# Kernel optimization log

Measured on AMD Instinct MI355X. Metric: run time of the kernel, lower is better.

Reference implementation:

```python
import jax, jax.numpy as jnp
import numpy as np

SHIFTS = [1, 3, 5, 7]
C = 16  # in_channels // 4
# -1 neighbor offsets for tmp1..tmp8 (dy, dx) in units of the dilation
OFFSETS = [(-1, -1), (-1, 0), (-1, 1), (0, 1), (1, 1), (1, 0), (1, -1), (0, -1)]


def setup_inputs() -> dict:
    key = jax.random.key(0)
    ks = jax.random.split(key, 32)
    d = {}
    d['cen'] = jax.random.normal(ks[0], (8, 64, 256, 256), jnp.float32)
    d['mas'] = jax.random.normal(ks[1], (8, 1, 256, 256), jnp.float32)
    d['in_conv_w'] = jax.random.normal(ks[2], (16, 64), jnp.float32) * 0.1
    d['in_conv_b'] = jax.random.normal(ks[3], (16,), jnp.float32) * 0.1
    for i, s in enumerate(SHIFTS):
        d[f'dw_w{s}'] = jax.random.normal(ks[4 + 2 * i], (16, 1, s, s), jnp.float32) * 0.1
        d[f'dw_b{s}'] = jax.random.normal(ks[5 + 2 * i], (16,), jnp.float32) * 0.1
    d['l1_w'] = jax.random.normal(ks[12], (4, 16, 4), jnp.float32) * 0.1
    d['l1_b'] = jax.random.normal(ks[13], (4, 16), jnp.float32) * 0.1
    d['l2_w'] = jax.random.normal(ks[14], (4, 16, 8), jnp.float32) * 0.1
    d['l2_b'] = jax.random.normal(ks[15], (4, 16), jnp.float32) * 0.1
    d['base_w'] = jax.random.normal(ks[16], (16, 4), jnp.float32) * 0.1
    d['bn_scale'] = jnp.ones((16,), jnp.float32)
    d['bn_bias'] = jnp.zeros((16,), jnp.float32)
    d['final_w'] = jax.random.normal(ks[17], (1, 16), jnp.float32) * 0.1
    d['final_b'] = jax.random.normal(ks[18], (1,), jnp.float32) * 0.1
    return d


def _dw_conv(x, w, b, pad):
    # depthwise conv, groups == channels
    y = jax.lax.conv_general_dilated(
        x, w, window_strides=(1, 1), padding=[(pad, pad), (pad, pad)],
        dimension_numbers=('NCHW', 'OIHW', 'NCHW'), feature_group_count=x.shape[1])
    return y + b[None, :, None, None]


def _shifted(x, dy, dx, d):
    # zero-padded shift: out(y,x) = in(y+dy, x+dx)
    H, W = x.shape[2], x.shape[3]
    p = jnp.pad(x, ((0, 0), (0, 0), (d, d), (d, d)))
    return p[:, :, d + dy:d + dy + H, d + dx:d + dx + W]


def _circ_shift(x, dw_w, dw_b, w1, b1, w2, b2, shift):
    x = _dw_conv(x, dw_w, dw_b, shift // 2)
    # tmp_k = x - x shifted by the k-th neighbor offset (dilation = shift)
    T = [x - _shifted(x, dy * shift, dx * shift, shift) for dy, dx in OFFSETS]
    # paired sums: S[k] = tmp_{k+1} + tmp_{k+5} (S repeats with period 4)
    S = [T[k] + T[k + 4] for k in range(4)]
    outs = []
    for k in range(8):  # fixed small structural loop
        feats = jnp.stack([S[(k + 1) % 4], S[(k + 3) % 4], S[(k + 2) % 4],
                           2.0 * T[(k + 4) % 8]], axis=2)  # (B,C,4,H,W)
        # grouped 1x1 conv (groups=C, 4C->C) == per-channel contraction over feature axis
        o = jnp.einsum('bcfhw,cf->bchw', feats, w1) + b1[None, :, None, None]
        outs.append(o * T[k])
    O = jnp.sort(jnp.stack(outs, axis=2), axis=2)  # (B,C,8,H,W) sorted over branch axis
    return jnp.einsum('bcfhw,cf->bchw', O, w2) + b2[None, :, None, None]


def reference(cen, mas, in_conv_w, in_conv_b, dw_w1, dw_b1, dw_w3, dw_b3,
              dw_w5, dw_b5, dw_w7, dw_b7, l1_w, l1_b, l2_w, l2_b,
              base_w, bn_scale, bn_bias, final_w, final_b):
    # in_conv: 1x1, in_channels -> C
    x = jnp.einsum('bihw,oi->bohw', cen, in_conv_w) + in_conv_b[None, :, None, None]
    dws = [(dw_w1, dw_b1), (dw_w3, dw_b3), (dw_w5, dw_b5), (dw_w7, dw_b7)]
    branches = [
        _circ_shift(x, dws[i][0], dws[i][1], l1_w[i], l1_b[i], l2_w[i], l2_b[i], SHIFTS[i])
        for i in range(len(SHIFTS))
    ]
    A = jnp.sort(jnp.stack(branches, axis=2), axis=2)  # (B,C,4,H,W)
    # out_conv: grouped 1x1 BaseConv (conv no-bias + BN(affine) + SiLU), then 1x1 -> 1, sigmoid
    y = jnp.einsum('bcfhw,cf->bchw', A, base_w)
    y = jax.nn.silu(y * bn_scale[None, :, None, None] + bn_bias[None, :, None, None])
    y = jnp.einsum('bchw,oc->bohw', y, final_w) + final_b[None, :, None, None]
    return jax.nn.sigmoid(y)
```

## Files before the change

### kernel.cpp

```cpp
#include <hip/hip_runtime.h>
#include <hip/hip_fp16.h>
#include <math.h>

#define HW 65536

typedef float v2f __attribute__((ext_vector_type(2), aligned(4)));
typedef _Float16 h2 __attribute__((ext_vector_type(2)));

__global__ __launch_bounds__(256, 8) void k_inconv(const float* __restrict__ cen,
                                                   const float* __restrict__ w,
                                                   const float* __restrict__ bias,
                                                   float* __restrict__ x) {
    int px = blockIdx.x * 256 + threadIdx.x;
    int b  = px >> 16;
    int hw = px & 65535;

    const float* src = cen + (long)(b * 64) * HW + hw;
    float acc[16];
#pragma unroll
    for (int o = 0; o < 16; o++) acc[o] = bias[o];

#pragma unroll 4
    for (int i = 0; i < 64; i++) {
        float v = src[(long)i * HW];
#pragma unroll
        for (int o = 0; o < 16; o++) acc[o] = fmaf(v, w[o * 64 + i], acc[o]);
    }
    float* dst = x + (long)(b * 16) * HW + hw;
#pragma unroll
    for (int o = 0; o < 16; o++) dst[(long)o * HW] = acc[o];
}

#define CEH(a, b) { h2 _t = __builtin_elementwise_min(a, b); \
                    b = __builtin_elementwise_max(a, b); a = _t; }

__device__ __forceinline__ void sort8_h2(h2* v) {
    CEH(v[0], v[1]); CEH(v[2], v[3]); CEH(v[4], v[5]); CEH(v[6], v[7]);
    CEH(v[0], v[2]); CEH(v[1], v[3]); CEH(v[4], v[6]); CEH(v[5], v[7]);
    CEH(v[1], v[2]); CEH(v[5], v[6]); CEH(v[0], v[4]); CEH(v[3], v[7]);
    CEH(v[1], v[5]); CEH(v[2], v[6]);
    CEH(v[1], v[4]); CEH(v[3], v[6]);
    CEH(v[2], v[4]); CEH(v[3], v[5]);
    CEH(v[3], v[4]);
}
__device__ __forceinline__ void sort4_h2(h2* v) {
    CEH(v[0], v[1]); CEH(v[2], v[3]); CEH(v[0], v[2]); CEH(v[1], v[3]); CEH(v[1], v[2]);
}

#define LXS 56
#define SS  48

__global__ __launch_bounds__(512, 4) void k_main(
    const float* __restrict__ x,
    const float* __restrict__ dw_w1, const float* __restrict__ dw_b1,
    const float* __restrict__ dw_w3, const float* __restrict__ dw_b3,
    const float* __restrict__ dw_w5, const float* __restrict__ dw_b5,
    const float* __restrict__ dw_w7, const float* __restrict__ dw_b7,
    const float* __restrict__ l1w, const float* __restrict__ l1b,
    const float* __restrict__ l2w, const float* __restrict__ l2b,
    const float* __restrict__ bw,  const float* __restrict__ bns,
    const float* __restrict__ bnb, __half* __restrict__ y16) {

    const int plane = blockIdx.y;
    const int c     = plane & 15;
    const int ty0   = (blockIdx.x >> 3) * 32;
    const int tx0   = (blockIdx.x & 7) * 32;
    const int tid   = threadIdx.x;

    __shared__ float lx[52 * LXS];
    __shared__ float lxs[4][46 * SS];

    const float* xp = x + (long)plane * HW;

    for (int i = tid; i < 52 * 52; i += 512) {
        int r  = i / 52;
        int cc = i - r * 52;
        int gy = ty0 - 10 + r, gx = tx0 - 10 + cc;
        float v = 0.f;
        if ((unsigned)gy < 256u && (unsigned)gx < 256u) v = xp[gy * 256 + gx];
        lx[r * LXS + cc] = v;
    }
    __syncthreads();

    const float* W7 = dw_w7 + c * 49;
    const float* W5 = dw_w5 + c * 25;
    const float* W3 = dw_w3 + c * 9;
    const float  W1 = dw_w1[c];
    const float  B1 = dw_b1[c], B3 = dw_b3[c], B5 = dw_b5[c], B7 = dw_b7[c];

    for (int u = tid; u < 46 * 23; u += 512) {
        int row = u / 23;
        int pc0 = (u - row * 23) * 2;
        v2f c7 = {0, 0}, c5 = {0, 0}, c3 = {0, 0}, c1 = {0, 0};
#pragma unroll
        for (int a = 0; a < 7; a++) {
            const float* rp = &lx[(row + a) * LXS + pc0];
            v2f q0 = *(const v2f*)rp;
            v2f q1 = *(const v2f*)(rp + 2);
            v2f q2 = *(const v2f*)(rp + 4);
            v2f q3 = *(const v2f*)(rp + 6);
            float v8 = rp[8];
            float v[9] = {q0.x, q0.y, q1.x, q1.y, q2.x, q2.y, q3.x, q3.y, v8};
#pragma unroll
            for (int bb = 0; bb < 7; bb++) {
                v2f vv = {v[bb], v[bb + 1]};
                c7 += vv * W7[a * 7 + bb];
            }
            if (a >= 1 && a <= 5) {
#pragma unroll
                for (int bb = 0; bb < 5; bb++) {
                    v2f vv = {v[bb + 1], v[bb + 2]};
                    c5 += vv * W5[(a - 1) * 5 + bb];
                }
            }
            if (a >= 2 && a <= 4) {
#pragma unroll
                for (int bb = 0; bb < 3; bb++) {
                    v2f vv = {v[bb + 2], v[bb + 3]};
                    c3 += vv * W3[(a - 2) * 3 + bb];
                }
            }
            if (a == 3) {
                v2f vv = {v[3], v[4]};
                c1 = vv * W1;
            }
        }
        int gy  = ty0 - 7 + row;
        int gx0 = tx0 - 7 + pc0;
        bool rin = ((unsigned)gy < 256u);
        bool in0 = rin && ((unsigned)gx0 < 256u);
        bool in1 = rin && ((unsigned)(gx0 + 1) < 256u);
        int o = row * SS + pc0;
        v2f s;
        s.x = in0 ? c1.x + B1 : 0.f; s.y = in1 ? c1.y + B1 : 0.f;
        *(v2f*)&lxs[0][o] = s;
        s.x = in0 ? c3.x + B3 : 0.f; s.y = in1 ? c3.y + B3 : 0.f;
        *(v2f*)&lxs[1][o] = s;
        s.x = in0 ? c5.x + B5 : 0.f; s.y = in1 ? c5.y + B5 : 0.f;
        *(v2f*)&lxs[2][o] = s;
        s.x = in0 ? c7.x + B7 : 0.f; s.y = in1 ? c7.y + B7 : 0.f;
        *(v2f*)&lxs[3][o] = s;
    }
    __syncthreads();

    const int ty  = tid >> 4;
    const int tx2 = (tid & 15) * 2;
    const int gy  = ty0 + ty, gx = tx0 + tx2;
    const int corner = ty * SS + tx2;

    v2f br[4];
#pragma unroll
    for (int i = 0; i < 4; i++) {
        const int s = 1 + 2 * i;
        const float* xs = lxs[i];
        v2f ctr = *(const v2f*)&xs[corner + 7 * SS + 7];
        v2f n0  = *(const v2f*)&xs[corner + (7 - s) * SS + (7 - s)];
        v2f n1  = *(const v2f*)&xs[corner + (7 - s) * SS + 7];
        v2f n2  = *(const v2f*)&xs[corner + (7 - s) * SS + (7 + s)];
        v2f n3  = *(const v2f*)&xs[corner + 7 * SS + (7 + s)];
        v2f n4  = *(const v2f*)&xs[corner + (7 + s) * SS + (7 + s)];
        v2f n5  = *(const v2f*)&xs[corner + (7 + s) * SS + 7];
        v2f n6  = *(const v2f*)&xs[corner + (7 + s) * SS + (7 - s)];
        v2f n7  = *(const v2f*)&xs[corner + 7 * SS + (7 - s)];

        v2f T[8];
        T[0] = ctr - n0; T[1] = ctr - n1; T[2] = ctr - n2; T[3] = ctr - n3;
        T[4] = ctr - n4; T[5] = ctr - n5; T[6] = ctr - n6; T[7] = ctr - n7;
        v2f S[4];
#pragma unroll
        for (int k = 0; k < 4; k++) S[k] = T[k] + T[k + 4];

        const float w10   = l1w[i * 64 + c * 4 + 0];
        const float w11   = l1w[i * 64 + c * 4 + 1];
        const float w12   = l1w[i * 64 + c * 4 + 2];
        const float w13x2 = 2.f * l1w[i * 64 + c * 4 + 3];
        const float bb1   = l1b[i * 16 + c];

        v2f R[4];
#pragma unroll
        for (int m = 0; m < 4; m++) {
            v2f r = S[(m + 2) & 3] * w12 + bb1;
            r = S[(m + 3) & 3] * w11 + r;
            r = S[(m + 1) & 3] * w10 + r;
            R[m] = r;
        }

        h2 h8[8];
#pragma unroll
        for (int k = 0; k < 8; k++) {
            v2f o = (T[(k + 4) & 7] * w13x2 + R[k & 3]) * T[k];
            h8[k] = __builtin_convertvector(o, h2);
        }
        sort8_h2(h8);

        v2f acc = {l2b[i * 16 + c], l2b[i * 16 + c]};
#pragma unroll
        for (int k = 0; k < 8; k++) {
            v2f ov = __builtin_convertvector(h8[k], v2f);
            acc += ov * l2w[i * 128 + c * 8 + k];
        }
        br[i] = acc;
    }

    h2 bh[4];
#pragma unroll
    for (int i = 0; i < 4; i++) bh[i] = __builtin_convertvector(br[i], h2);
    sort4_h2(bh);

    v2f yv = {0.f, 0.f};
#pragma unroll
    for (int i = 0; i < 4; i++) {
        v2f bv = __builtin_convertvector(bh[i], v2f);
        yv += bv * bw[c * 4 + i];
    }
    const float bsc = bns[c], bbi = bnb[c];
    float zx = fmaf(yv.x, bsc, bbi);
    float zy = fmaf(yv.y, bsc, bbi);
    float sx = zx / (1.f + __expf(-zx));
    float sy = zy / (1.f + __expf(-zy));
    *(__half2*)&y16[(long)plane * HW + gy * 256 + gx] = __floats2half2_rn(sx, sy);
}

__global__ __launch_bounds__(256) void k_final(const __half* __restrict__ y16,
                                               const float* __restrict__ fw,
                                               const float* __restrict__ fb,
                                               float* __restrict__ out) {
    long t  = (long)blockIdx.x * 256 + threadIdx.x;
    long p0 = t * 2;
    int  b  = (int)(p0 >> 16);
    int  hw = (int)(p0 & 65535);

    float accx = fb[0], accy = fb[0];
#pragma unroll
    for (int cc = 0; cc < 16; cc++) {
        __half2 h = *(const __half2*)(y16 + (long)(b * 16 + cc) * HW + hw);
        float2 v = __half22float2(h);
        float wv = fw[cc];
        accx = fmaf(v.x, wv, accx);
        accy = fmaf(v.y, wv, accy);
    }
    float2 r;
    r.x = 1.f / (1.f + __expf(-accx));
    r.y = 1.f / (1.f + __expf(-accy));
    *(float2*)(out + p0) = r;
}

extern "C" void kernel_launch(void* const* d_in, const int* in_sizes, int n_in,
                              void* d_out, int out_size, void* d_ws, size_t ws_size,
                              hipStream_t stream) {
    (void)in_sizes; (void)n_in; (void)out_size; (void)ws_size;
    const float* cen   = (const float*)d_in[0];
    const float* in_w  = (const float*)d_in[2];
    const float* in_b  = (const float*)d_in[3];
    const float* dw_w1 = (const float*)d_in[4];
    const float* dw_b1 = (const float*)d_in[5];
    const float* dw_w3 = (const float*)d_in[6];
    const float* dw_b3 = (const float*)d_in[7];
    const float* dw_w5 = (const float*)d_in[8];
    const float* dw_b5 = (const float*)d_in[9];
    const float* dw_w7 = (const float*)d_in[10];
    const float* dw_b7 = (const float*)d_in[11];
    const float* l1w   = (const float*)d_in[12];
    const float* l1b   = (const float*)d_in[13];
    const float* l2w   = (const float*)d_in[14];
    const float* l2b   = (const float*)d_in[15];
    const float* bw    = (const float*)d_in[16];
    const float* bns   = (const float*)d_in[17];
    const float* bnb   = (const float*)d_in[18];
    const float* fw    = (const float*)d_in[19];
    const float* fb    = (const float*)d_in[20];

    float*  xbuf = (float*)d_ws;
    __half* y16  = (__half*)(xbuf + (size_t)8 * 16 * HW);
    float*  out  = (float*)d_out;

    k_inconv<<<2048, 256, 0, stream>>>(cen, in_w, in_b, xbuf);
    k_main<<<dim3(64, 128), 512, 0, stream>>>(xbuf, dw_w1, dw_b1, dw_w3, dw_b3,
                                              dw_w5, dw_b5, dw_w7, dw_b7,
                                              l1w, l1b, l2w, l2b, bw, bns, bnb, y16);
    k_final<<<1024, 256, 0, stream>>>(y16, fw, fb, out);
}
```

Baseline: 394.4 us.

## Vectorize inconv with LDS weights, pad LDS strides, use fp16 branch accumulation

The 1x1 input conv now stages its weights and bias in shared memory and has each thread handle two pixels with float2 loads and stores, halving the grid. In the main kernel the LDS row strides become odd (53/47) to reduce bank conflicts, and the depthwise conv loop is rewritten with scalar fmaf and scalar stores instead of packed v2f. The per-branch l2 accumulation and the base_w combine now run in packed fp16 instead of fp32. This cuts ALU work but adds rounding error, and the odd strides break 8-byte alignment for the v2f LDS reads.

Measured after the change: 398.1 us. No clear change (+0.9%).

```diff
diff --git a/kernel.cpp b/kernel.cpp
--- a/kernel.cpp
+++ b/kernel.cpp
@@ -7,28 +7,40 @@
 typedef float v2f __attribute__((ext_vector_type(2), aligned(4)));
 typedef _Float16 h2 __attribute__((ext_vector_type(2)));
 
-__global__ __launch_bounds__(256, 8) void k_inconv(const float* __restrict__ cen,
-                                                   const float* __restrict__ w,
-                                                   const float* __restrict__ bias,
-                                                   float* __restrict__ x) {
-    int px = blockIdx.x * 256 + threadIdx.x;
-    int b  = px >> 16;
-    int hw = px & 65535;
-
-    const float* src = cen + (long)(b * 64) * HW + hw;
-    float acc[16];
-#pragma unroll
-    for (int o = 0; o < 16; o++) acc[o] = bias[o];
-
-#pragma unroll 4
+__global__ __launch_bounds__(256) void k_inconv(const float* __restrict__ cen,
+                                                const float* __restrict__ w,
+                                                const float* __restrict__ bias,
+                                                float* __restrict__ x) {
+    __shared__ float sw[1024];
+    __shared__ float sb[16];
+    int tid = threadIdx.x;
+    for (int i = tid; i < 1024; i += 256) sw[i] = w[i];
+    if (tid < 16) sb[tid] = bias[tid];
+    __syncthreads();
+
+    long t  = (long)blockIdx.x * 256 + tid;
+    long p0 = t * 2;
+    int  b  = (int)(p0 >> 16);
+    int  hw = (int)(p0 & 65535);
+
+    const float2* src = (const float2*)(cen + ((long)b * 64) * HW + hw);
+    float2 acc[16];
+#pragma unroll
+    for (int o = 0; o < 16; o++) { float bv = sb[o]; acc[o] = make_float2(bv, bv); }
+
+#pragma unroll 8
     for (int i = 0; i < 64; i++) {
-        float v = src[(long)i * HW];
-#pragma unroll
-        for (int o = 0; o < 16; o++) acc[o] = fmaf(v, w[o * 64 + i], acc[o]);
-    }
-    float* dst = x + (long)(b * 16) * HW + hw;
-#pragma unroll
-    for (int o = 0; o < 16; o++) dst[(long)o * HW] = acc[o];
+        float2 v = src[(long)i * (HW / 2)];
+#pragma unroll
+        for (int o = 0; o < 16; o++) {
+            float wv = sw[o * 64 + i];
+            acc[o].x = fmaf(v.x, wv, acc[o].x);
+            acc[o].y = fmaf(v.y, wv, acc[o].y);
+        }
+    }
+    float2* dst = (float2*)(x + ((long)b * 16) * HW + hw);
+#pragma unroll
+    for (int o = 0; o < 16; o++) dst[(long)o * (HW / 2)] = acc[o];
 }
 
 #define CEH(a, b) { h2 _t = __builtin_elementwise_min(a, b); \
@@ -47,8 +59,8 @@
     CEH(v[0], v[1]); CEH(v[2], v[3]); CEH(v[0], v[2]); CEH(v[1], v[3]); CEH(v[1], v[2]);
 }
 
-#define LXS 56
-#define SS  48
+#define LXS 53
+#define SS  47
 
 __global__ __launch_bounds__(512, 4) void k_main(
     const float* __restrict__ x,
@@ -91,38 +103,29 @@
     for (int u = tid; u < 46 * 23; u += 512) {
         int row = u / 23;
         int pc0 = (u - row * 23) * 2;
-        v2f c7 = {0, 0}, c5 = {0, 0}, c3 = {0, 0}, c1 = {0, 0};
+        float c7[2] = {0, 0}, c5[2] = {0, 0}, c3[2] = {0, 0}, c1[2] = {0, 0};
 #pragma unroll
         for (int a = 0; a < 7; a++) {
             const float* rp = &lx[(row + a) * LXS + pc0];
-            v2f q0 = *(const v2f*)rp;
-            v2f q1 = *(const v2f*)(rp + 2);
-            v2f q2 = *(const v2f*)(rp + 4);
-            v2f q3 = *(const v2f*)(rp + 6);
-            float v8 = rp[8];
-            float v[9] = {q0.x, q0.y, q1.x, q1.y, q2.x, q2.y, q3.x, q3.y, v8};
-#pragma unroll
-            for (int bb = 0; bb < 7; bb++) {
-                v2f vv = {v[bb], v[bb + 1]};
-                c7 += vv * W7[a * 7 + bb];
-            }
-            if (a >= 1 && a <= 5) {
-#pragma unroll
-                for (int bb = 0; bb < 5; bb++) {
-                    v2f vv = {v[bb + 1], v[bb + 2]};
-                    c5 += vv * W5[(a - 1) * 5 + bb];
+            float v[9];
+#pragma unroll
+            for (int j = 0; j < 9; j++) v[j] = rp[j];
+#pragma unroll
+            for (int j = 0; j < 2; j++) {
+#pragma unroll
+                for (int bb = 0; bb < 7; bb++)
+                    c7[j] = fmaf(v[j + bb], W7[a * 7 + bb], c7[j]);
+                if (a >= 1 && a <= 5) {
+#pragma unroll
+                    for (int bb = 0; bb < 5; bb++)
+                        c5[j] = fmaf(v[j + 1 + bb], W5[(a - 1) * 5 + bb], c5[j]);
                 }
-            }
-            if (a >= 2 && a <= 4) {
-#pragma unroll
-                for (int bb = 0; bb < 3; bb++) {
-                    v2f vv = {v[bb + 2], v[bb + 3]};
-                    c3 += vv * W3[(a - 2) * 3 + bb];
+                if (a >= 2 && a <= 4) {
+#pragma unroll
+                    for (int bb = 0; bb < 3; bb++)
+                        c3[j] = fmaf(v[j + 2 + bb], W3[(a - 2) * 3 + bb], c3[j]);
                 }
-            }
-            if (a == 3) {
-                v2f vv = {v[3], v[4]};
-                c1 = vv * W1;
+                if (a == 3) c1[j] = v[j + 3] * W1;
             }
         }
         int gy  = ty0 - 7 + row;
@@ -131,15 +134,14 @@
         bool in0 = rin && ((unsigned)gx0 < 256u);
         bool in1 = rin && ((unsigned)(gx0 + 1) < 256u);
         int o = row * SS + pc0;
-        v2f s;
-        s.x = in0 ? c1.x + B1 : 0.f; s.y = in1 ? c1.y + B1 : 0.f;
-        *(v2f*)&lxs[0][o] = s;
-        s.x = in0 ? c3.x + B3 : 0.f; s.y = in1 ? c3.y + B3 : 0.f;
-        *(v2f*)&lxs[1][o] = s;
-        s.x = in0 ? c5.x + B5 : 0.f; s.y = in1 ? c5.y + B5 : 0.f;
-        *(v2f*)&lxs[2][o] = s;
-        s.x = in0 ? c7.x + B7 : 0.f; s.y = in1 ? c7.y + B7 : 0.f;
-        *(v2f*)&lxs[3][o] = s;
+        lxs[0][o]     = in0 ? c1[0] + B1 : 0.f;
+        lxs[0][o + 1] = in1 ? c1[1] + B1 : 0.f;
+        lxs[1][o]     = in0 ? c3[0] + B3 : 0.f;
+        lxs[1][o + 1] = in1 ? c3[1] + B3 : 0.f;
+        lxs[2][o]     = in0 ? c5[0] + B5 : 0.f;
+        lxs[2][o + 1] = in1 ? c5[1] + B5 : 0.f;
+        lxs[3][o]     = in0 ? c7[0] + B7 : 0.f;
+        lxs[3][o + 1] = in1 ? c7[1] + B7 : 0.f;
     }
     __syncthreads();
 
@@ -148,7 +150,7 @@
     const int gy  = ty0 + ty, gx = tx0 + tx2;
     const int corner = ty * SS + tx2;
 
-    v2f br[4];
+    h2 brh[4];
 #pragma unroll
     for (int i = 0; i < 4; i++) {
         const int s = 1 + 2 * i;
@@ -193,29 +195,28 @@
         }
         sort8_h2(h8);
 
-        v2f acc = {l2b[i * 16 + c], l2b[i * 16 + c]};
+        _Float16 l2bh = (_Float16)l2b[i * 16 + c];
+        h2 acc = {l2bh, l2bh};
 #pragma unroll
         for (int k = 0; k < 8; k++) {
-            v2f ov = __builtin_convertvector(h8[k], v2f);
-            acc += ov * l2w[i * 128 + c * 8 + k];
-        }
-        br[i] = acc;
-    }
-
-    h2 bh[4];
-#pragma unroll
-    for (int i = 0; i < 4; i++) bh[i] = __builtin_convertvector(br[i], h2);
-    sort4_h2(bh);
-
-    v2f yv = {0.f, 0.f};
+            _Float16 wh = (_Float16)l2w[i * 128 + c * 8 + k];
+            h2 wv = {wh, wh};
+            acc = h8[k] * wv + acc;
+        }
+        brh[i] = acc;
+    }
+
+    sort4_h2(brh);
+    h2 yvh = {(_Float16)0.f, (_Float16)0.f};
 #pragma unroll
     for (int i = 0; i < 4; i++) {
-        v2f bv = __builtin_convertvector(bh[i], v2f);
-        yv += bv * bw[c * 4 + i];
+        _Float16 bwh = (_Float16)bw[c * 4 + i];
+        h2 bv = {bwh, bwh};
+        yvh = brh[i] * bv + yvh;
     }
     const float bsc = bns[c], bbi = bnb[c];
-    float zx = fmaf(yv.x, bsc, bbi);
-    float zy = fmaf(yv.y, bsc, bbi);
+    float zx = fmaf((float)yvh.x, bsc, bbi);
+    float zy = fmaf((float)yvh.y, bsc, bbi);
     float sx = zx / (1.f + __expf(-zx));
     float sy = zy / (1.f + __expf(-zy));
     *(__half2*)&y16[(long)plane * HW + gy * 256 + gx] = __floats2half2_rn(sx, sy);
@@ -274,7 +275,7 @@
     __half* y16  = (__half*)(xbuf + (size_t)8 * 16 * HW);
     float*  out  = (float*)d_out;
 
-    k_inconv<<<2048, 256, 0, stream>>>(cen, in_w, in_b, xbuf);
+    k_inconv<<<1024, 256, 0, stream>>>(cen, in_w, in_b, xbuf);
     k_main<<<dim3(64, 128), 512, 0, stream>>>(xbuf, dw_w1, dw_b1, dw_w3, dw_b3,
                                               dw_w5, dw_b5, dw_w7, dw_b7,
                                               l1w, l1b, l2w, l2b, bw, bns, bnb, y16);
```
